# Kernel tuning notes

Hardware: AMD Instinct MI355X
Metric: run time of the kernel (lower is better)

Reference implementation:

```python
import jax, jax.numpy as jnp
import numpy as np

B, SEQ, PRED, DM = 16, 2048, 2048, 64
P = SEQ + PRED            # PointNum = 4096, per-node feature length
NLAYER, HID = 3, 4096     # MLPNums, ggdmodel hidden sizes
NH, HS = 16, 4096         # NumAttentionHeads, HiddenSize
G_CONST, K = 1.0, 8
NN = DM * DM              # 4096 == P, MHSA input dim (required by original code)


def setup_inputs() -> dict:
    key = jax.random.key(0)
    ks = jax.random.split(key, 11)
    s_mlp = 1.0 / np.sqrt(P).astype(np.float32)
    s_att = 1.0 / np.sqrt(NN).astype(np.float32)
    s_out = 1.0 / np.sqrt(HS).astype(np.float32)
    return {
        "x": jax.random.normal(ks[0], (B, P, DM), jnp.float32),
        "W_mlp": jax.random.normal(ks[1], (NLAYER, P, HID), jnp.float32) * s_mlp,
        "b_mlp": jnp.zeros((NLAYER, HID), jnp.float32),
        "Wq": jax.random.normal(ks[2], (NN, HS), jnp.float32) * s_att,
        "bq": jnp.zeros((HS,), jnp.float32),
        "Wk": jax.random.normal(ks[3], (NN, HS), jnp.float32) * s_att,
        "bk": jnp.zeros((HS,), jnp.float32),
        "Wv": jax.random.normal(ks[4], (NN, HS), jnp.float32) * s_att,
        "bv": jnp.zeros((HS,), jnp.float32),
        "Wo": jax.random.normal(ks[5], (HS, HS), jnp.float32) * s_out,
        "bo": jnp.zeros((HS,), jnp.float32),
    }


def _grav_adj(h):
    # h: [B, N, D] node features -> symmetrized, top-K masked gravity adjacency [B, N, N]
    norm = jnp.linalg.norm(h, axis=-1)                      # [B, N]
    m = jnp.sum(h, axis=-1) / norm                          # node "mass"
    sim = jnp.einsum('bnd,bmd->bnm', h, h) / (norm[:, :, None] * norm[:, None, :])
    F = G_CONST * m[:, :, None] * m[:, None, :] * sim * sim  # gravity matrix
    kth = jax.lax.top_k(F, K)[0][..., -1:]                  # per-row Kth largest value
    F = jnp.where(F >= kth, F, 0.0)                         # keep only top-K per row
    F = jnp.maximum(F, 0.0)                                 # ReLU
    return 0.5 * (F + jnp.swapaxes(F, -1, -2))              # symmetrize


def reference(x, W_mlp, b_mlp, Wq, bq, Wk, bk, Wv, bv, Wo, bo):
    h = jnp.swapaxes(x, 1, 2)                               # [B, N=DM, P]
    adjs = [_grav_adj(h)]
    for l in range(NLAYER):                                 # each MLP applied to the same h
        hv = h @ W_mlp[l] + b_mlp[l]                        # [B, N, HID]
        adjs.append(_grav_adj(hv))
    A = jnp.stack(adjs, axis=1)                             # [B, L, N, N], L = NLAYER + 1
    Lseq = A.shape[1]
    tok = A.reshape(B, Lseq, NN)                            # L tokens of dim N*N
    dh = HS // NH
    q = (tok @ Wq + bq).reshape(B, Lseq, NH, dh)
    k = (tok @ Wk + bk).reshape(B, Lseq, NH, dh)
    v = (tok @ Wv + bv).reshape(B, Lseq, NH, dh)
    scores = jnp.einsum('blhd,bmhd->bhlm', q, k) / np.sqrt(dh).astype(np.float32)
    attn = jax.nn.softmax(scores, axis=-1)
    ctx = jnp.einsum('bhlm,bmhd->blhd', attn, v).reshape(B, Lseq, HS)
    out = ctx @ Wo + bo                                     # [B, L, HS]
    return jnp.where(out > 0.5, out, 0.0)
```

## Files before the change

kernel.cpp:

```cpp
#include <hip/hip_runtime.h>
#include <math.h>


#define B16 16
#define PDIM 4096
#define NNODE 64
#define NCHUNK 32
#define KCG 128

typedef __attribute__((ext_vector_type(8))) short bf16x8;
typedef __attribute__((ext_vector_type(4))) float f32x4;
typedef __attribute__((ext_vector_type(4))) unsigned short us4;
typedef __attribute__((ext_vector_type(8))) unsigned short us8;

__device__ inline void split2(float x, unsigned short& h, unsigned short& l) {
  unsigned u = __float_as_uint(x);
  unsigned hu = (u + 0x7fffu + ((u >> 16) & 1u)) & 0xffff0000u;
  h = (unsigned short)(hu >> 16);
  float lo = x - __uint_as_float(hu);
  unsigned u2 = __float_as_uint(lo);
  l = (unsigned short)((u2 + 0x7fffu + ((u2 >> 16) & 1u)) >> 16);
}

__device__ inline void gload16(const void* g, void* lds) {
  __builtin_amdgcn_global_load_lds((const unsigned int*)g, (unsigned int*)lds, 16, 0, 0);
}

__global__ __launch_bounds__(256) void k_transpose(const float* __restrict__ x,
                                                   float* __restrict__ h,
                                                   unsigned short* __restrict__ AhT,
                                                   unsigned short* __restrict__ AlT,
                                                   int mode) {
  __shared__ float t[64][65];
  int b = blockIdx.y;
  int p0 = blockIdx.x * 64;
  const float* xb = x + (size_t)b * PDIM * NNODE;
#pragma unroll
  for (int i = 0; i < 16; ++i) {
    int e = i * 256 + threadIdx.x;
    int p = e >> 6, n = e & 63;
    t[p][n] = xb[(size_t)p0 * 64 + e];
  }
  __syncthreads();
  if (mode != 2) {
    float* hb = h + (size_t)b * NNODE * PDIM;
#pragma unroll
    for (int i = 0; i < 16; ++i) {
      int e = i * 256 + threadIdx.x;
      int n = e >> 6, p = e & 63;
      hb[(size_t)n * PDIM + p0 + p] = t[p][n];
    }
  }
  if (mode == 0) return;
#pragma unroll
  for (int j = 0; j < 2; ++j) {
    int cid = j * 256 + threadIdx.x;
    int n2 = cid >> 3, kg8 = cid & 7;
    us8 hv_, lv_;
#pragma unroll
    for (int e = 0; e < 8; ++e) {
      unsigned short hh, ll;
      split2(t[kg8 * 8 + e][n2], hh, ll);
      hv_[e] = hh; lv_[e] = ll;
    }
    int m = b * 64 + n2;
    int ks = (p0 >> 5) + (kg8 >> 2);
    size_t idx = (((size_t)(m >> 7) * 128 + ks) * 8 + ((m >> 4) & 7)) * 512 +
                 (size_t)((n2 & 15) + 16 * (kg8 & 3)) * 8;
    *(us8*)&AhT[idx] = hv_;
    *(us8*)&AlT[idx] = lv_;
  }
}

__global__ __launch_bounds__(512) void k_gemm_mlpf(
    const unsigned short* __restrict__ Ah, const unsigned short* __restrict__ Al,
    const float* __restrict__ W, float* __restrict__ Cp) {
  __shared__ unsigned short sAh[2][4096], sAl[2][4096];
  __shared__ unsigned short sBh[2][4096], sBl[2][4096];
  int tid = threadIdx.x;
  int l = tid & 63, wid = tid >> 6;
  int wr = wid >> 2, wc = wid & 3;
  int nb = blockIdx.x, mb = blockIdx.y, z = blockIdx.z;
  const int spp = 64;
  int ks0 = z * spp;

  size_t abase = ((size_t)mb * 128 + ks0) * 4096 + tid * 8;

  const float* wbase = W + (size_t)((l >> 4) * 8) * 4096 + nb * 128 + wid * 16 + (l & 15);
  int sidx = wid * 512 + l * 8;

  f32x4 acc[4][2];
#pragma unroll
  for (int i = 0; i < 4; ++i)
#pragma unroll
    for (int j = 0; j < 2; ++j) acc[i][j] = (f32x4){0.f, 0.f, 0.f, 0.f};

  gload16(Ah + abase, &sAh[0][tid * 8]);
  gload16(Al + abase, &sAl[0][tid * 8]);
  {
    us8 hi, lo;
#pragma unroll
    for (int e = 0; e < 8; ++e) {
      unsigned short hh, ll;
      split2(wbase[(size_t)ks0 * 131072 + (size_t)e * 4096], hh, ll);
      hi[e] = hh; lo[e] = ll;
    }
    *(us8*)&sBh[0][sidx] = hi;
    *(us8*)&sBl[0][sidx] = lo;
  }
  __syncthreads();

  int buf = 0;
  for (int t = 0; t < spp; ++t) {
    bool more = (t + 1 < spp);
    float wv[8];
    if (more) {
      size_t off = abase + (size_t)(t + 1) * 4096;
      gload16(Ah + off, &sAh[buf ^ 1][tid * 8]);
      gload16(Al + off, &sAl[buf ^ 1][tid * 8]);
      size_t wo = (size_t)(ks0 + t + 1) * 131072;
#pragma unroll
      for (int e = 0; e < 8; ++e) wv[e] = wbase[wo + (size_t)e * 4096];
    }
    bf16x8 ah[4], al4[4], bh2[2], bl2[2];
#pragma unroll
    for (int i = 0; i < 4; ++i) {
      ah[i]  = *(const bf16x8*)&sAh[buf][(wr * 4 + i) * 512 + l * 8];
      al4[i] = *(const bf16x8*)&sAl[buf][(wr * 4 + i) * 512 + l * 8];
    }
#pragma unroll
    for (int j = 0; j < 2; ++j) {
      bh2[j] = *(const bf16x8*)&sBh[buf][(wc * 2 + j) * 512 + l * 8];
      bl2[j] = *(const bf16x8*)&sBl[buf][(wc * 2 + j) * 512 + l * 8];
    }
#pragma unroll
    for (int mt = 0; mt < 4; ++mt)
#pragma unroll
      for (int nt = 0; nt < 2; ++nt) {
        acc[mt][nt] = __builtin_amdgcn_mfma_f32_16x16x32_bf16(ah[mt],  bh2[nt], acc[mt][nt], 0, 0, 0);
        acc[mt][nt] = __builtin_amdgcn_mfma_f32_16x16x32_bf16(ah[mt],  bl2[nt], acc[mt][nt], 0, 0, 0);
        acc[mt][nt] = __builtin_amdgcn_mfma_f32_16x16x32_bf16(al4[mt], bh2[nt], acc[mt][nt], 0, 0, 0);
      }
    if (more) {
      us8 hi, lo;
#pragma unroll
      for (int e = 0; e < 8; ++e) {
        unsigned short hh, ll;
        split2(wv[e], hh, ll);
        hi[e] = hh; lo[e] = ll;
      }
      *(us8*)&sBh[buf ^ 1][sidx] = hi;
      *(us8*)&sBl[buf ^ 1][sidx] = lo;
    }
    __syncthreads();
    buf ^= 1;
  }

  int n0 = nb * 128, m0 = mb * 128;
  float* Cz = Cp + (size_t)z * 4194304;
#pragma unroll
  for (int mt = 0; mt < 4; ++mt)
#pragma unroll
    for (int nt = 0; nt < 2; ++nt) {
      int col = n0 + wc * 32 + nt * 16 + (l & 15);
      int rowb = m0 + wr * 64 + mt * 16 + ((l >> 4) << 2);
#pragma unroll
      for (int r = 0; r < 4; ++r)
        Cz[(size_t)(rowb + r) * 4096 + col] = acc[mt][nt][r];
    }
}

__global__ __launch_bounds__(512) void k_gemm_wsf32(
    const unsigned short* __restrict__ Ah, const unsigned short* __restrict__ Al,
    const float* __restrict__ W0, const float* __restrict__ W1,
    const float* __restrict__ W2, float* __restrict__ Cp, int ksplit) {
  __shared__ unsigned short sAh[2][2048], sAl[2][2048];
  __shared__ unsigned short sBh[2][4096], sBl[2][4096];
  int tid = threadIdx.x;
  int l = tid & 63, wid = tid >> 6;
  int wr = wid >> 2, wc = wid & 3;
  int nb = blockIdx.x, z = blockIdx.z;
  int mat = z / ksplit, kz = z - mat * ksplit;
  const float* W = (mat == 0) ? W0 : ((mat == 1) ? W1 : W2);
  int nsteps = 128 / ksplit;
  int ks0 = kz * nsteps;
  int n0 = nb * 128;

  const float* wbase = W + (size_t)((l >> 4) * 8) * 4096 + n0 + wid * 16 + (l & 15);
  int sidx = wid * 512 + l * 8;

  f32x4 acc[2][2];
#pragma unroll
  for (int i = 0; i < 2; ++i)
#pragma unroll
    for (int j = 0; j < 2; ++j) acc[i][j] = (f32x4){0.f, 0.f, 0.f, 0.f};

  {
    if (tid < 256) gload16(Ah + (size_t)ks0 * 4096 + tid * 8, &sAh[0][tid * 8]);
    else           gload16(Al + (size_t)ks0 * 4096 + (tid - 256) * 8, &sAl[0][(tid - 256) * 8]);
    float wv[8];
#pragma unroll
    for (int e = 0; e < 8; ++e) wv[e] = wbase[(size_t)ks0 * 131072 + (size_t)e * 4096];
    us8 hi, lo;
#pragma unroll
    for (int e = 0; e < 8; ++e) {
      unsigned short hh, ll;
      split2(wv[e], hh, ll);
      hi[e] = hh; lo[e] = ll;
    }
    *(us8*)&sBh[0][sidx] = hi;
    *(us8*)&sBl[0][sidx] = lo;
  }
  __syncthreads();

  int buf = 0;
  for (int t = 0; t < nsteps; ++t) {
    bool more = (t + 1 < nsteps);
    float wv[8];
    if (more) {
      int ks = ks0 + t + 1;
      if (tid < 256) gload16(Ah + (size_t)ks * 4096 + tid * 8, &sAh[buf ^ 1][tid * 8]);
      else           gload16(Al + (size_t)ks * 4096 + (tid - 256) * 8, &sAl[buf ^ 1][(tid - 256) * 8]);
#pragma unroll
      for (int e = 0; e < 8; ++e) wv[e] = wbase[(size_t)ks * 131072 + (size_t)e * 4096];
    }
    bf16x8 aH[2], aL[2], bH[2], bL[2];
#pragma unroll
    for (int i = 0; i < 2; ++i) {
      aH[i] = *(const bf16x8*)&sAh[buf][(wr * 2 + i) * 512 + l * 8];
      aL[i] = *(const bf16x8*)&sAl[buf][(wr * 2 + i) * 512 + l * 8];
      bH[i] = *(const bf16x8*)&sBh[buf][(wc * 2 + i) * 512 + l * 8];
      bL[i] = *(const bf16x8*)&sBl[buf][(wc * 2 + i) * 512 + l * 8];
    }
#pragma unroll
    for (int i = 0; i < 2; ++i)
#pragma unroll
      for (int j = 0; j < 2; ++j) {
        acc[i][j] = __builtin_amdgcn_mfma_f32_16x16x32_bf16(aH[i], bH[j], acc[i][j], 0, 0, 0);
        acc[i][j] = __builtin_amdgcn_mfma_f32_16x16x32_bf16(aH[i], bL[j], acc[i][j], 0, 0, 0);
        acc[i][j] = __builtin_amdgcn_mfma_f32_16x16x32_bf16(aL[i], bH[j], acc[i][j], 0, 0, 0);
      }
    if (more) {
      us8 hi, lo;
#pragma unroll
      for (int e = 0; e < 8; ++e) {
        unsigned short hh, ll;
        split2(wv[e], hh, ll);
        hi[e] = hh; lo[e] = ll;
      }
      *(us8*)&sBh[buf ^ 1][sidx] = hi;
      *(us8*)&sBl[buf ^ 1][sidx] = lo;
    }
    __syncthreads();
    buf ^= 1;
  }

  float* Cz = Cp + (size_t)z * 262144;
#pragma unroll
  for (int i = 0; i < 2; ++i)
#pragma unroll
    for (int j = 0; j < 2; ++j) {
      int col = n0 + wc * 32 + j * 16 + (l & 15);
#pragma unroll
      for (int r = 0; r < 4; ++r) {
        int row = (wr * 2 + i) * 16 + ((l >> 4) << 2) + r;
        Cz[(size_t)row * 4096 + col] = acc[i][j][r];
      }
    }
}

__global__ __launch_bounds__(256) void k_gram_fuse(
    const float* __restrict__ Cp, const float* __restrict__ bias,
    float* __restrict__ Gp, float* __restrict__ Sp, int nparts) {
  __shared__ unsigned short sZh[2048], sZl[2048];
  int zk = blockIdx.x, b = blockIdx.y;
  int tid = threadIdx.x;
  int l = tid & 63, w = tid >> 6;
  int srow = tid >> 2, skq = tid & 3;
  const float* cbase = Cp + (size_t)(b * 64 + srow) * 4096;
  int swidx = (srow >> 4) * 512 + (skq * 16 + (srow & 15)) * 8;

  f32x4 acc[4], racc;
#pragma unroll
  for (int j = 0; j < 4; ++j) acc[j] = (f32x4){0.f, 0.f, 0.f, 0.f};
  racc = (f32x4){0.f, 0.f, 0.f, 0.f};
  bf16x8 ones;
#pragma unroll
  for (int e = 0; e < 8; ++e) ones[e] = (short)0x3F80;

  for (int s = 0; s < 8; ++s) {
    int k0 = zk * 256 + s * 32 + skq * 8;
    float v[8];
#pragma unroll
    for (int e = 0; e < 8; ++e) v[e] = bias[k0 + e];
    for (int p = 0; p < nparts; ++p) {
      const float* pp = cbase + (size_t)p * 4194304 + k0;
      float4 a0 = *(const float4*)pp;
      float4 a1 = *(const float4*)(pp + 4);
      v[0] += a0.x; v[1] += a0.y; v[2] += a0.z; v[3] += a0.w;
      v[4] += a1.x; v[5] += a1.y; v[6] += a1.z; v[7] += a1.w;
    }
    us8 hi, lo;
#pragma unroll
    for (int e = 0; e < 8; ++e) {
      unsigned short hh, ll;
      split2(v[e], hh, ll);
      hi[e] = hh; lo[e] = ll;
    }
    *(us8*)&sZh[swidx] = hi;
    *(us8*)&sZl[swidx] = lo;
    __syncthreads();
    bf16x8 bh[4], bl4[4];
#pragma unroll
    for (int nt = 0; nt < 4; ++nt) {
      bh[nt]  = *(const bf16x8*)&sZh[nt * 512 + l * 8];
      bl4[nt] = *(const bf16x8*)&sZl[nt * 512 + l * 8];
    }
    bf16x8 ah = bh[w], al = bl4[w];
#pragma unroll
    for (int nt = 0; nt < 4; ++nt) {
      acc[nt] = __builtin_amdgcn_mfma_f32_16x16x32_bf16(ah, bh[nt], acc[nt], 0, 0, 0);
      acc[nt] = __builtin_amdgcn_mfma_f32_16x16x32_bf16(ah, bl4[nt], acc[nt], 0, 0, 0);
      acc[nt] = __builtin_amdgcn_mfma_f32_16x16x32_bf16(al, bh[nt], acc[nt], 0, 0, 0);
    }
    racc = __builtin_amdgcn_mfma_f32_16x16x32_bf16(ah, ones, racc, 0, 0, 0);
    racc = __builtin_amdgcn_mfma_f32_16x16x32_bf16(al, ones, racc, 0, 0, 0);
    __syncthreads();
  }

  float* Gz = Gp + ((size_t)zk * B16 + b) * 4096;
#pragma unroll
  for (int nt = 0; nt < 4; ++nt) {
    int col = nt * 16 + (l & 15);
#pragma unroll
    for (int r = 0; r < 4; ++r) {
      int row = w * 16 + ((l >> 4) << 2) + r;
      Gz[row * 64 + col] = acc[nt][r];
    }
  }
  if ((l & 15) == 0) {
    float* Sz = Sp + ((size_t)zk * B16 + b) * 64;
#pragma unroll
    for (int r = 0; r < 4; ++r) Sz[w * 16 + ((l >> 4) << 2) + r] = racc[r];
  }
}

__global__ __launch_bounds__(256) void k_gram_mfma(
    const unsigned short* __restrict__ Zh, const unsigned short* __restrict__ Zl,
    float* __restrict__ Gp, float* __restrict__ Sp,
    int bs1, int ks_stride, int nsteps) {
  __shared__ unsigned short sZh[2][2048], sZl[2][2048];
  int z = blockIdx.x, b = blockIdx.y;
  int tid = threadIdx.x;
  int l = tid & 63, w = tid >> 6;
  size_t zbase = (size_t)(b >> 1) * 524288 + (size_t)(b & 1) * bs1;
  int ks0 = z * nsteps;

  f32x4 acc[4], racc;
#pragma unroll
  for (int j = 0; j < 4; ++j) acc[j] = (f32x4){0.f, 0.f, 0.f, 0.f};
  racc = (f32x4){0.f, 0.f, 0.f, 0.f};
  bf16x8 ones;
#pragma unroll
  for (int e = 0; e < 8; ++e) ones[e] = (short)0x3F80;

  gload16(Zh + zbase + (size_t)ks0 * ks_stride + tid * 8, &sZh[0][tid * 8]);
  gload16(Zl + zbase + (size_t)ks0 * ks_stride + tid * 8, &sZl[0][tid * 8]);
  __syncthreads();

  int buf = 0;
  for (int t = 0; t < nsteps; ++t) {
    if (t + 1 < nsteps) {
      size_t off = zbase + (size_t)(ks0 + t + 1) * ks_stride + tid * 8;
      gload16(Zh + off, &sZh[buf ^ 1][tid * 8]);
      gload16(Zl + off, &sZl[buf ^ 1][tid * 8]);
    }
    bf16x8 bh[4], bl4[4];
#pragma unroll
    for (int nt = 0; nt < 4; ++nt) {
      bh[nt]  = *(const bf16x8*)&sZh[buf][nt * 512 + l * 8];
      bl4[nt] = *(const bf16x8*)&sZl[buf][nt * 512 + l * 8];
    }
    bf16x8 ah = bh[w], al = bl4[w];
#pragma unroll
    for (int nt = 0; nt < 4; ++nt) {
      acc[nt] = __builtin_amdgcn_mfma_f32_16x16x32_bf16(ah, bh[nt], acc[nt], 0, 0, 0);
      acc[nt] = __builtin_amdgcn_mfma_f32_16x16x32_bf16(ah, bl4[nt], acc[nt], 0, 0, 0);
      acc[nt] = __builtin_amdgcn_mfma_f32_16x16x32_bf16(al, bh[nt], acc[nt], 0, 0, 0);
    }
    racc = __builtin_amdgcn_mfma_f32_16x16x32_bf16(ah, ones, racc, 0, 0, 0);
    racc = __builtin_amdgcn_mfma_f32_16x16x32_bf16(al, ones, racc, 0, 0, 0);
    __syncthreads();
    buf ^= 1;
  }

  float* Gz = Gp + ((size_t)z * B16 + b) * 4096;
#pragma unroll
  for (int nt = 0; nt < 4; ++nt) {
    int col = nt * 16 + (l & 15);
#pragma unroll
    for (int r = 0; r < 4; ++r) {
      int row = w * 16 + ((l >> 4) << 2) + r;
      Gz[row * 64 + col] = acc[nt][r];
    }
  }
  if ((l & 15) == 0) {
    float* Sz = Sp + ((size_t)z * B16 + b) * 64;
#pragma unroll
    for (int r = 0; r < 4; ++r) Sz[w * 16 + ((l >> 4) << 2) + r] = racc[r];
  }
}

__global__ __launch_bounds__(256) void k_gred(const float* __restrict__ Gp,
                                              const float* __restrict__ Sp,
                                              float* __restrict__ G,
                                              float* __restrict__ S, int slot, int nc) {
  int idx = blockIdx.x * 256 + threadIdx.x;
  if (idx < 65536) {
    float s = 0.f;
    for (int c = 0; c < nc; ++c) s += Gp[(size_t)c * 65536 + idx];
    G[(size_t)slot * 65536 + idx] = s;
  } else if (idx < 66560) {
    int i2 = idx - 65536;
    float s = 0.f;
    for (int c = 0; c < nc; ++c) s += Sp[(size_t)c * 1024 + i2];
    S[(size_t)slot * 1024 + i2] = s;
  }
}

__global__ __launch_bounds__(256) void k_redqkv8(const float* __restrict__ Cp,
                                                 const float* __restrict__ bq,
                                                 const float* __restrict__ bk,
                                                 const float* __restrict__ bv,
                                                 float* __restrict__ q,
                                                 float* __restrict__ k,
                                                 float* __restrict__ v) {
  int idx = blockIdx.x * 256 + threadIdx.x;
  int mat = idx >> 18;
  int rn = idx & ((1 << 18) - 1);
  int n = rn & 4095;
  const float* base = Cp + (size_t)mat * 8 * 262144;
  float s = 0.f;
#pragma unroll
  for (int p = 0; p < 8; ++p) s += base[(size_t)p * 262144 + rn];
  if (mat == 0) q[rn] = s + bq[n];
  else if (mat == 1) k[rn] = s + bk[n];
  else v[rn] = s + bv[n];
}

__global__ __launch_bounds__(256) void k_redN(const float* __restrict__ Cp,
                                              const float* __restrict__ bias,
                                              float* __restrict__ dst,
                                              int nparts, int thr) {
  int idx = blockIdx.x * 256 + threadIdx.x;
  float s = bias[idx & 4095];
  for (int p = 0; p < nparts; ++p) s += Cp[(size_t)p * 262144 + idx];
  if (thr) s = (s > 0.5f) ? s : 0.f;
  dst[idx] = s;
}

__device__ inline float wmax64(float v) {
#pragma unroll
  for (int off = 32; off; off >>= 1) v = fmaxf(v, __shfl_xor(v, off));
  return v;
}

__global__ __launch_bounds__(256) void k_adj_t(const float* __restrict__ G,
                                               const float* __restrict__ S,
                                               unsigned short* __restrict__ tokh,
                                               unsigned short* __restrict__ tokl) {
  __shared__ float Fm[64][64];
  __shared__ float nrm[64], mm[64];
  int b = blockIdx.x >> 2, lz = blockIdx.x & 3;
  int tid = threadIdx.x;
  int j = tid & 63, w = tid >> 6;
  const float* Gb = G + ((size_t)lz * B16 + b) * 4096;
  const float* Sb = S + ((size_t)lz * B16 + b) * 64;
  if (tid < 64) {
    float nj = sqrtf(Gb[tid * 64 + tid]);
    nrm[tid] = nj;
    mm[tid] = Sb[tid] / nj;
  }
  __syncthreads();
  for (int i = w; i < 64; i += 4) {
    float g = Gb[i * 64 + j];
    float sim = g / (nrm[i] * nrm[j]);
    Fm[i][j] = mm[i] * mm[j] * sim * sim;
  }
  __syncthreads();
  for (int i = w; i < 64; i += 4) {
    float f = Fm[i][j];
    int cnt = 0;
#pragma unroll
    for (int u4 = 0; u4 < 16; ++u4) {
      float4 q = *(const float4*)&Fm[i][u4 * 4];
      cnt += (q.x > f) + (q.y > f) + (q.z > f) + (q.w > f);
    }
    float cand = (cnt <= 7) ? f : INFINITY;
#pragma unroll
    for (int off = 32; off; off >>= 1) cand = fminf(cand, __shfl_xor(cand, off));
    float fm = (f >= cand) ? fmaxf(f, 0.f) : 0.f;
    Fm[i][j] = fm;
  }
  __syncthreads();
  int r = b * 4 + lz;
  int mt = r >> 4, rl = r & 15;
#pragma unroll
  for (int c = 0; c < 2; ++c) {
    int cid = tid * 2 + c;
    int jj0 = cid >> 3, g = cid & 7;
    us8 hv_, lv_;
#pragma unroll
    for (int e = 0; e < 8; ++e) {
      int kcol = g * 8 + e;
      float val = 0.5f * (Fm[jj0][kcol] + Fm[kcol][jj0]);
      unsigned short hh, ll;
      split2(val, hh, ll);
      hv_[e] = hh; lv_[e] = ll;
    }
    int ks = jj0 * 2 + (g >> 2);
    size_t idx = ((size_t)ks * 8 + mt) * 512 + (size_t)(rl + 16 * (g & 3)) * 8;
    *(us8*)&tokh[idx] = hv_;
    *(us8*)&tokl[idx] = lv_;
  }
}

__global__ __launch_bounds__(64) void k_attn_t(const float* __restrict__ q,
                                               const float* __restrict__ k,
                                               const float* __restrict__ v,
                                               unsigned short* __restrict__ ctxh,
                                               unsigned short* __restrict__ ctxl) {
  __shared__ float cb[4][256];
  int hd = blockIdx.x, b = blockIdx.y;
  int t = threadIdx.x;
  float qr[4][4], kr[4][4], vr[4][4];
#pragma unroll
  for (int l = 0; l < 4; ++l)
#pragma unroll
    for (int s = 0; s < 4; ++s) {
      size_t off = ((size_t)(b * 4 + l)) * 4096 + hd * 256 + t + s * 64;
      qr[l][s] = q[off]; kr[l][s] = k[off]; vr[l][s] = v[off];
    }
  float sc[4][4];
#pragma unroll
  for (int l = 0; l < 4; ++l)
#pragma unroll
    for (int m = 0; m < 4; ++m) {
      float p = 0.f;
#pragma unroll
      for (int s = 0; s < 4; ++s) p = fmaf(qr[l][s], kr[m][s], p);
#pragma unroll
      for (int off = 32; off; off >>= 1) p += __shfl_xor(p, off);
      sc[l][m] = p * (1.0f / 16.0f);
    }
  float at[4][4];
#pragma unroll
  for (int l = 0; l < 4; ++l) {
    float mx = fmaxf(fmaxf(sc[l][0], sc[l][1]), fmaxf(sc[l][2], sc[l][3]));
    float e0 = expf(sc[l][0] - mx), e1 = expf(sc[l][1] - mx);
    float e2 = expf(sc[l][2] - mx), e3 = expf(sc[l][3] - mx);
    float d = e0 + e1 + e2 + e3;
    at[l][0] = e0 / d; at[l][1] = e1 / d; at[l][2] = e2 / d; at[l][3] = e3 / d;
  }
#pragma unroll
  for (int l = 0; l < 4; ++l)
#pragma unroll
    for (int s = 0; s < 4; ++s) {
      float c = 0.f;
#pragma unroll
      for (int m = 0; m < 4; ++m) c = fmaf(at[l][m], vr[m][s], c);
      cb[l][s * 64 + t] = c;
    }
  __syncthreads();
  int lq = t >> 4, c16 = t & 15;
  int mt = b >> 2, rl = (b & 3) * 4 + lq;
#pragma unroll
  for (int e8 = 0; e8 < 2; ++e8) {
    us8 hv_, lv_;
#pragma unroll
    for (int e = 0; e < 8; ++e) {
      unsigned short hh, ll;
      split2(cb[lq][c16 * 16 + e8 * 8 + e], hh, ll);
      hv_[e] = hh; lv_[e] = ll;
    }
    int ks = hd * 8 + (c16 >> 1);
    size_t idx = ((size_t)ks * 8 + mt) * 512 + (size_t)(rl + 16 * ((c16 * 2 + e8) & 3)) * 8;
    *(us8*)&ctxh[idx] = hv_;
    *(us8*)&ctxl[idx] = lv_;
  }
}

__global__ __launch_bounds__(256) void k_gram_partial(const float* __restrict__ Z,
                                                      float* __restrict__ Gp,
                                                      float* __restrict__ Sp) {
  __shared__ float Zt[KCG][68];
  int c = blockIdx.x, b = blockIdx.y;
  int tid = threadIdx.x;
  const float* Zb = Z + (size_t)b * NNODE * PDIM + c * KCG;
#pragma unroll
  for (int i = 0; i < 32; ++i) {
    int e = i * 256 + tid;
    int r = e >> 7, kk = e & 127;
    Zt[kk][r] = Zb[(size_t)r * PDIM + kk];
  }
  __syncthreads();
  int ii = tid >> 2, j0 = (tid & 3) << 4;
  float acc[16] = {};
  for (int kk = 0; kk < KCG; ++kk) {
    float zi = Zt[kk][ii];
    float4 z0 = *(const float4*)&Zt[kk][j0 + 0];
    float4 z1 = *(const float4*)&Zt[kk][j0 + 4];
    float4 z2 = *(const float4*)&Zt[kk][j0 + 8];
    float4 z3 = *(const float4*)&Zt[kk][j0 + 12];
    acc[0] = fmaf(zi, z0.x, acc[0]);   acc[1] = fmaf(zi, z0.y, acc[1]);
    acc[2] = fmaf(zi, z0.z, acc[2]);   acc[3] = fmaf(zi, z0.w, acc[3]);
    acc[4] = fmaf(zi, z1.x, acc[4]);   acc[5] = fmaf(zi, z1.y, acc[5]);
    acc[6] = fmaf(zi, z1.z, acc[6]);   acc[7] = fmaf(zi, z1.w, acc[7]);
    acc[8] = fmaf(zi, z2.x, acc[8]);   acc[9] = fmaf(zi, z2.y, acc[9]);
    acc[10] = fmaf(zi, z2.z, acc[10]); acc[11] = fmaf(zi, z2.w, acc[11]);
    acc[12] = fmaf(zi, z3.x, acc[12]); acc[13] = fmaf(zi, z3.y, acc[13]);
    acc[14] = fmaf(zi, z3.z, acc[14]); acc[15] = fmaf(zi, z3.w, acc[15]);
  }
  float* gp = Gp + ((size_t)c * B16 + b) * 4096 + ii * 64 + j0;
#pragma unroll
  for (int j = 0; j < 16; ++j) gp[j] = acc[j];
  if (tid < 64) {
    float s = 0.f;
    for (int kk = 0; kk < KCG; ++kk) s += Zt[kk][tid];
    Sp[((size_t)c * B16 + b) * 64 + tid] = s;
  }
}

__global__ __launch_bounds__(256) void k_gram_reduce(const float* __restrict__ Gp,
                                                     const float* __restrict__ Sp,
                                                     float* __restrict__ G,
                                                     float* __restrict__ S, int slot) {
  int idx = blockIdx.x * 256 + threadIdx.x;
  if (idx < B16 * 4096) {
    float s = 0.f;
    for (int c = 0; c < NCHUNK; ++c) s += Gp[(size_t)c * (B16 * 4096) + idx];
    G[(size_t)slot * (B16 * 4096) + idx] = s;
  } else {
    int idx2 = idx - B16 * 4096;
    float s = 0.f;
    for (int c = 0; c < NCHUNK; ++c) s += Sp[(size_t)c * (B16 * 64) + idx2];
    S[(size_t)slot * (B16 * 64) + idx2] = s;
  }
}

__global__ __launch_bounds__(256) void k_gemm_mfma(
    const float* __restrict__ A, const float* __restrict__ B0,
    const float* __restrict__ B1, const float* __restrict__ B2,
    const float* __restrict__ bias, float* __restrict__ C,
    int mrows, int mstore, int N, int K, int ksplit) {
  __shared__ __align__(16) unsigned short sA[2][8][64][8];
  __shared__ __align__(16) unsigned short sB[2][8][64][8];
  int z = blockIdx.z;
  int mat = z / ksplit, ks = z - mat * ksplit;
  const float* Bm = (mat == 0) ? B0 : ((mat == 1) ? B1 : B2);
  int kchunk = K / ksplit;
  int k0 = ks * kchunk, k1 = k0 + kchunk;
  int tid = threadIdx.x;
  int l = tid & 63;
  int wr = (tid >> 7) & 1, wc = (tid >> 6) & 1;
  int m0 = blockIdx.y * 128, n0g = blockIdx.x * 128;
  bool activeM = (m0 + wr * 64) < mstore;
  int am = tid >> 1;
  int arow = m0 + am; if (arow >= mrows) arow = mrows - 1;
  const float* Arow = A + (size_t)arow * K;
  int amt = am >> 4;
  int bk = tid >> 3;
  int bnb = (tid & 7) * 4;
  int bg = bk >> 3, bslot = bk & 7;
  f32x4 acc[4][4];
#pragma unroll
  for (int i = 0; i < 4; ++i)
#pragma unroll
    for (int j = 0; j < 4; ++j) acc[i][j] = (f32x4){0.f, 0.f, 0.f, 0.f};
  for (int kb = k0; kb < k1; kb += 32) {
    __syncthreads();
#pragma unroll
    for (int i = 0; i < 4; ++i) {
      int kq = (tid & 1) * 4 + i * 8;
      float4 a = *(const float4*)(Arow + kb + kq);
      unsigned short h0, h1, h2, h3, l0, l1, l2, l3;
      split2(a.x, h0, l0); split2(a.y, h1, l1);
      split2(a.z, h2, l2); split2(a.w, h3, l3);
      int lane_t = (am & 15) + 16 * (kq >> 3);
      int sb = kq & 4;
      *(us4*)&sA[0][amt][lane_t][sb] = (us4){h0, h1, h2, h3};
      *(us4*)&sA[1][amt][lane_t][sb] = (us4){l0, l1, l2, l3};
    }
    {
      const float* Brow = Bm + (size_t)(kb + bk) * N + n0g;
#pragma unroll
      for (int i = 0; i < 4; ++i) {
        int n = bnb + i * 32;
        int nt = n >> 4, nr = n & 15;
        float4 b = *(const float4*)(Brow + n);
        float be[4] = {b.x, b.y, b.z, b.w};
#pragma unroll
        for (int e = 0; e < 4; ++e) {
          unsigned short hh, ll;
          split2(be[e], hh, ll);
          sB[0][nt][nr + e + 16 * bg][bslot] = hh;
          sB[1][nt][nr + e + 16 * bg][bslot] = ll;
        }
      }
    }
    __syncthreads();
    if (!activeM) continue;
    bf16x8 ah[4], al[4], bh[4], bl[4];
#pragma unroll
    for (int t = 0; t < 4; ++t) {
      ah[t] = *(const bf16x8*)&sA[0][wr * 4 + t][l][0];
      al[t] = *(const bf16x8*)&sA[1][wr * 4 + t][l][0];
      bh[t] = *(const bf16x8*)&sB[0][wc * 4 + t][l][0];
      bl[t] = *(const bf16x8*)&sB[1][wc * 4 + t][l][0];
    }
#pragma unroll
    for (int mt = 0; mt < 4; ++mt)
#pragma unroll
      for (int nt = 0; nt < 4; ++nt) {
        acc[mt][nt] = __builtin_amdgcn_mfma_f32_16x16x32_bf16(ah[mt], bh[nt], acc[mt][nt], 0, 0, 0);
        acc[mt][nt] = __builtin_amdgcn_mfma_f32_16x16x32_bf16(ah[mt], bl[nt], acc[mt][nt], 0, 0, 0);
        acc[mt][nt] = __builtin_amdgcn_mfma_f32_16x16x32_bf16(al[mt], bh[nt], acc[mt][nt], 0, 0, 0);
      }
  }
  if (!activeM) return;
  float* Cz = C + (size_t)z * mstore * N;
#pragma unroll
  for (int mt = 0; mt < 4; ++mt)
#pragma unroll
    for (int nt = 0; nt < 4; ++nt) {
      int col = n0g + wc * 64 + nt * 16 + (l & 15);
      float badd = bias ? bias[col] : 0.f;
#pragma unroll
      for (int r = 0; r < 4; ++r) {
        int row = m0 + wr * 64 + mt * 16 + ((l >> 4) << 2) + r;
        if (row < mstore) Cz[(size_t)row * N + col] = acc[mt][nt][r] + badd;
      }
    }
}

__global__ __launch_bounds__(64) void k_adj_fb(const float* __restrict__ G,
                                               const float* __restrict__ S,
                                               float* __restrict__ tok) {
  __shared__ float Fm[64][64];
  __shared__ float nrm[64], mm[64];
  int b = blockIdx.x >> 2, lz = blockIdx.x & 3;
  int j = threadIdx.x;
  const float* Gb = G + ((size_t)lz * B16 + b) * 4096;
  const float* Sb = S + ((size_t)lz * B16 + b) * 64;
  float nj = sqrtf(Gb[j * 64 + j]);
  nrm[j] = nj;
  mm[j] = Sb[j] / nj;
  __syncthreads();
  for (int i = 0; i < 64; ++i) {
    float g = Gb[i * 64 + j];
    float sim = g / (nrm[i] * nj);
    float F = mm[i] * mm[j] * sim * sim;
    float v = F;
    bool act = true;
    float kth = 0.f;
#pragma unroll
    for (int it = 0; it < 8; ++it) {
      float mv = wmax64(act ? v : -INFINITY);
      kth = mv;
      unsigned long long ball = __ballot(act && (v == mv));
      int first = __ffsll(ball) - 1;
      if (j == first) act = false;
    }
    float fm = (F >= kth) ? F : 0.f;
    Fm[i][j] = fmaxf(fm, 0.f);
  }
  __syncthreads();
  float* tb = tok + ((size_t)b * 4 + lz) * 4096;
  for (int i = 0; i < 64; ++i) tb[i * 64 + j] = 0.5f * (Fm[i][j] + Fm[j][i]);
}

__global__ __launch_bounds__(256) void k_qkv_reduce(const float* __restrict__ Cp,
                                                    const float* __restrict__ bq,
                                                    const float* __restrict__ bk,
                                                    const float* __restrict__ bv,
                                                    float* __restrict__ q,
                                                    float* __restrict__ k,
                                                    float* __restrict__ v) {
  int idx = blockIdx.x * 256 + threadIdx.x;
  int mat = idx >> 18;
  int rn = idx & ((1 << 18) - 1);
  int n = rn & 4095;
  const float* base = Cp + (size_t)mat * 4 * 262144;
  float s = base[rn] + base[rn + 262144] + base[rn + 2 * 262144] + base[rn + 3 * 262144];
  if (mat == 0) q[rn] = s + bq[n];
  else if (mat == 1) k[rn] = s + bk[n];
  else v[rn] = s + bv[n];
}

__global__ __launch_bounds__(64) void k_attn_fb(const float* __restrict__ q,
                                                const float* __restrict__ k,
                                                const float* __restrict__ v,
                                                float* __restrict__ ctx) {
  int hd = blockIdx.x, b = blockIdx.y;
  int t = threadIdx.x;
  float qr[4][4], kr[4][4], vr[4][4];
#pragma unroll
  for (int l = 0; l < 4; ++l)
#pragma unroll
    for (int s = 0; s < 4; ++s) {
      size_t off = ((size_t)(b * 4 + l)) * 4096 + hd * 256 + t + s * 64;
      qr[l][s] = q[off]; kr[l][s] = k[off]; vr[l][s] = v[off];
    }
  float sc[4][4];
#pragma unroll
  for (int l = 0; l < 4; ++l)
#pragma unroll
    for (int m = 0; m < 4; ++m) {
      float p = 0.f;
#pragma unroll
      for (int s = 0; s < 4; ++s) p = fmaf(qr[l][s], kr[m][s], p);
#pragma unroll
      for (int off = 32; off; off >>= 1) p += __shfl_xor(p, off);
      sc[l][m] = p * (1.0f / 16.0f);
    }
  float at[4][4];
#pragma unroll
  for (int l = 0; l < 4; ++l) {
    float mx = fmaxf(fmaxf(sc[l][0], sc[l][1]), fmaxf(sc[l][2], sc[l][3]));
    float e0 = expf(sc[l][0] - mx), e1 = expf(sc[l][1] - mx);
    float e2 = expf(sc[l][2] - mx), e3 = expf(sc[l][3] - mx);
    float d = e0 + e1 + e2 + e3;
    at[l][0] = e0 / d; at[l][1] = e1 / d; at[l][2] = e2 / d; at[l][3] = e3 / d;
  }
#pragma unroll
  for (int l = 0; l < 4; ++l)
#pragma unroll
    for (int s = 0; s < 4; ++s) {
      float c = 0.f;
#pragma unroll
      for (int m = 0; m < 4; ++m) c = fmaf(at[l][m], vr[m][s], c);
      ctx[((size_t)(b * 4 + l)) * 4096 + hd * 256 + t + s * 64] = c;
    }
}

__global__ __launch_bounds__(256) void k_out_reduce(const float* __restrict__ Cp,
                                                    const float* __restrict__ bo,
                                                    float* __restrict__ out) {
  int idx = blockIdx.x * 256 + threadIdx.x;
  int n = idx & 4095;
  float s = bo[n];
#pragma unroll
  for (int p = 0; p < 8; ++p) s += Cp[(size_t)p * 262144 + idx];
  out[idx] = (s > 0.5f) ? s : 0.f;
}

extern "C" void kernel_launch(void* const* d_in, const int* in_sizes, int n_in,
                              void* d_out, int out_size, void* d_ws, size_t ws_size,
                              hipStream_t stream) {
  const float* x     = (const float*)d_in[0];
  const float* W_mlp = (const float*)d_in[1];
  const float* b_mlp = (const float*)d_in[2];
  const float* Wq = (const float*)d_in[3]; const float* bq = (const float*)d_in[4];
  const float* Wk = (const float*)d_in[5]; const float* bk = (const float*)d_in[6];
  const float* Wv = (const float*)d_in[7]; const float* bv = (const float*)d_in[8];
  const float* Wo = (const float*)d_in[9]; const float* bo = (const float*)d_in[10];
  float* out = (float*)d_out;
  float* ws = (float*)d_ws;

  float* h   = ws;
  float* Gp  = ws + 8388608;
  float* Sp  = ws + 10485760;
  float* G   = ws + 10518528;
  float* S   = ws + 10780672;

  const size_t NEED = 50368512ull * 4ull;
  if (ws_size >= NEED) {
    float* q   = ws + 10784768;
    float* kk  = ws + 11046912;
    float* vv  = ws + 11309056;
    unsigned short* AhT = (unsigned short*)(ws + 11571200);
    unsigned short* AlT = (unsigned short*)(ws + 13668352);
    float* Cp           = ws + 32542720;
    unsigned short* tokh = (unsigned short*)(ws + 49319936);
    unsigned short* tokl = (unsigned short*)(ws + 49582080);
    unsigned short* ctxh = (unsigned short*)(ws + 49844224);
    unsigned short* ctxl = (unsigned short*)(ws + 50106368);

    k_transpose<<<dim3(64, 16), 256, 0, stream>>>(x, h, AhT, AlT, 2);

    k_gram_mfma<<<dim3(8, 16), 256, 0, stream>>>(AhT, AlT, Gp, Sp, 2048, 4096, 16);
    k_gred<<<260, 256, 0, stream>>>(Gp, Sp, G, S, 0, 8);

    for (int l = 0; l < 3; ++l) {
      k_gemm_mlpf<<<dim3(32, 8, 2), 512, 0, stream>>>(AhT, AlT,
                                                      W_mlp + (size_t)l * 16777216, Cp);
      k_gram_fuse<<<dim3(16, 16), 256, 0, stream>>>(Cp, b_mlp + (size_t)l * 4096,
                                                    Gp, Sp, 2);
      k_gred<<<260, 256, 0, stream>>>(Gp, Sp, G, S, l + 1, 16);
    }

    k_adj_t<<<64, 256, 0, stream>>>(G, S, tokh, tokl);

    k_gemm_wsf32<<<dim3(32, 1, 24), 512, 0, stream>>>(tokh, tokl, Wq, Wk, Wv, Cp, 8);
    k_redqkv8<<<3072, 256, 0, stream>>>(Cp, bq, bk, bv, q, kk, vv);

    k_attn_t<<<dim3(16, 16), 64, 0, stream>>>(q, kk, vv, ctxh, ctxl);

    k_gemm_wsf32<<<dim3(32, 1, 8), 512, 0, stream>>>(ctxh, ctxl, Wo, Wo, Wo, Cp, 8);
    k_redN<<<1024, 256, 0, stream>>>(Cp, bo, out, 8, 1);
  } else {
    float* hv  = ws + 4194304;
    float* tok = ws + 10784768;
    float* q   = ws + 11046912;
    float* kk  = ws + 11309056;
    float* vv  = ws + 11571200;
    float* ctx = ws + 11833344;
    float* qkvp = hv;
    float* op   = h;

    k_transpose<<<dim3(64, 16), 256, 0, stream>>>(x, h, (unsigned short*)0,
                                                  (unsigned short*)0, 0);
    k_gram_partial<<<dim3(NCHUNK, 16), 256, 0, stream>>>(h, Gp, Sp);
    k_gram_reduce<<<260, 256, 0, stream>>>(Gp, Sp, G, S, 0);
    for (int l = 0; l < 3; ++l) {
      const float* Wl = W_mlp + (size_t)l * PDIM * 4096;
      const float* bl = b_mlp + (size_t)l * 4096;
      k_gemm_mfma<<<dim3(32, 8, 1), 256, 0, stream>>>(h, Wl, Wl, Wl, bl, hv,
                                                      1024, 1024, 4096, 4096, 1);
      k_gram_partial<<<dim3(NCHUNK, 16), 256, 0, stream>>>(hv, Gp, Sp);
      k_gram_reduce<<<260, 256, 0, stream>>>(Gp, Sp, G, S, l + 1);
    }
    k_adj_fb<<<64, 64, 0, stream>>>(G, S, tok);
    k_gemm_mfma<<<dim3(32, 1, 12), 256, 0, stream>>>(tok, Wq, Wk, Wv, nullptr, qkvp,
                                                     64, 64, 4096, 4096, 4);
    k_qkv_reduce<<<3072, 256, 0, stream>>>(qkvp, bq, bk, bv, q, kk, vv);
    k_attn_fb<<<dim3(16, 16), 64, 0, stream>>>(q, kk, vv, ctx);
    k_gemm_mfma<<<dim3(32, 1, 8), 256, 0, stream>>>(ctx, Wo, Wo, Wo, nullptr, op,
                                                    64, 64, 4096, 4096, 8);
    k_out_reduce<<<1024, 256, 0, stream>>>(op, bo, out);
  }
}
```

Baseline: 593.1 us.

## Pre-split MLP weights into bf16 hi/lo tiles before a pure-async GEMM

Adds a separate k_wsplit kernel that converts each MLP weight matrix into pre-tiled bf16 hi/lo arrays. The GEMM can then stream both operands with async global-to-LDS loads instead of doing strided fp32 loads and splitting them inside the main loop. This removes conversion ALU work and register-staged B loads from the GEMM critical path. The cost is an extra pass per layer that reads 64MB of fp32 and writes 64MB of bf16, with the GEMM then reading that 64MB again.

```diff
diff --git a/kernel.cpp b/kernel.cpp
--- a/kernel.cpp
+++ b/kernel.cpp
@@ -72,22 +72,53 @@
   }
 }
 
-__global__ __launch_bounds__(512) void k_gemm_mlpf(
+__global__ __launch_bounds__(256) void k_wsplit(const float* __restrict__ W,
+                                                unsigned short* __restrict__ WhT,
+                                                unsigned short* __restrict__ WlT) {
+  __shared__ float Wt[32][132];
+  int nb = blockIdx.x, kb = blockIdx.y;
+  int tid = threadIdx.x;
+#pragma unroll
+  for (int i = 0; i < 4; ++i) {
+    int idx = i * 256 + tid;
+    int row = idx >> 5, c4 = idx & 31;
+    float4 v = *(const float4*)&W[(size_t)(kb * 32 + row) * 4096 + nb * 128 + c4 * 4];
+    *(float4*)&Wt[row][c4 * 4] = v;
+  }
+  __syncthreads();
+#pragma unroll
+  for (int j = 0; j < 2; ++j) {
+    int cid = j * 256 + tid;
+    int nl = cid & 127, kg = cid >> 7;
+    us8 hv_, lv_;
+#pragma unroll
+    for (int e = 0; e < 8; ++e) {
+      unsigned short hh, ll;
+      split2(Wt[kg * 8 + e][nl], hh, ll);
+      hv_[e] = hh; lv_[e] = ll;
+    }
+    size_t idx = (((size_t)nb * 128 + kb) * 8 + (nl >> 4)) * 512 +
+                 (size_t)((nl & 15) + 16 * kg) * 8;
+    *(us8*)&WhT[idx] = hv_;
+    *(us8*)&WlT[idx] = lv_;
+  }
+}
+
+__global__ __launch_bounds__(512) void k_gemm_bf16(
     const unsigned short* __restrict__ Ah, const unsigned short* __restrict__ Al,
-    const float* __restrict__ W, float* __restrict__ Cp) {
+    const unsigned short* __restrict__ Bh, const unsigned short* __restrict__ Bl,
+    float* __restrict__ Cp, int Ksteps, int ksplit, int N, int mstore) {
   __shared__ unsigned short sAh[2][4096], sAl[2][4096];
   __shared__ unsigned short sBh[2][4096], sBl[2][4096];
   int tid = threadIdx.x;
   int l = tid & 63, wid = tid >> 6;
   int wr = wid >> 2, wc = wid & 3;
   int nb = blockIdx.x, mb = blockIdx.y, z = blockIdx.z;
-  const int spp = 64;
+  int spp = Ksteps / ksplit;
   int ks0 = z * spp;
 
-  size_t abase = ((size_t)mb * 128 + ks0) * 4096 + tid * 8;
-
-  const float* wbase = W + (size_t)((l >> 4) * 8) * 4096 + nb * 128 + wid * 16 + (l & 15);
-  int sidx = wid * 512 + l * 8;
+  const size_t abase = ((size_t)mb * Ksteps + ks0) * 4096 + tid * 8;
+  const size_t bbase = ((size_t)nb * Ksteps + ks0) * 4096 + tid * 8;
 
   f32x4 acc[4][2];
 #pragma unroll
@@ -97,41 +128,29 @@
 
   gload16(Ah + abase, &sAh[0][tid * 8]);
   gload16(Al + abase, &sAl[0][tid * 8]);
-  {
-    us8 hi, lo;
-#pragma unroll
-    for (int e = 0; e < 8; ++e) {
-      unsigned short hh, ll;
-      split2(wbase[(size_t)ks0 * 131072 + (size_t)e * 4096], hh, ll);
-      hi[e] = hh; lo[e] = ll;
-    }
-    *(us8*)&sBh[0][sidx] = hi;
-    *(us8*)&sBl[0][sidx] = lo;
-  }
+  gload16(Bh + bbase, &sBh[0][tid * 8]);
+  gload16(Bl + bbase, &sBl[0][tid * 8]);
   __syncthreads();
 
   int buf = 0;
   for (int t = 0; t < spp; ++t) {
-    bool more = (t + 1 < spp);
-    float wv[8];
-    if (more) {
-      size_t off = abase + (size_t)(t + 1) * 4096;
-      gload16(Ah + off, &sAh[buf ^ 1][tid * 8]);
-      gload16(Al + off, &sAl[buf ^ 1][tid * 8]);
-      size_t wo = (size_t)(ks0 + t + 1) * 131072;
-#pragma unroll
-      for (int e = 0; e < 8; ++e) wv[e] = wbase[wo + (size_t)e * 4096];
+    if (t + 1 < spp) {
+      size_t off = (size_t)(t + 1) * 4096;
+      gload16(Ah + abase + off, &sAh[buf ^ 1][tid * 8]);
+      gload16(Al + abase + off, &sAl[buf ^ 1][tid * 8]);
+      gload16(Bh + bbase + off, &sBh[buf ^ 1][tid * 8]);
+      gload16(Bl + bbase + off, &sBl[buf ^ 1][tid * 8]);
     }
     bf16x8 ah[4], al4[4], bh2[2], bl2[2];
 #pragma unroll
-    for (int i = 0; i < 4; ++i) {
-      ah[i]  = *(const bf16x8*)&sAh[buf][(wr * 4 + i) * 512 + l * 8];
-      al4[i] = *(const bf16x8*)&sAl[buf][(wr * 4 + i) * 512 + l * 8];
-    }
-#pragma unroll
-    for (int j = 0; j < 2; ++j) {
-      bh2[j] = *(const bf16x8*)&sBh[buf][(wc * 2 + j) * 512 + l * 8];
-      bl2[j] = *(const bf16x8*)&sBl[buf][(wc * 2 + j) * 512 + l * 8];
+    for (int mt = 0; mt < 4; ++mt) {
+      ah[mt]  = *(const bf16x8*)&sAh[buf][(wr * 4 + mt) * 512 + l * 8];
+      al4[mt] = *(const bf16x8*)&sAl[buf][(wr * 4 + mt) * 512 + l * 8];
+    }
+#pragma unroll
+    for (int nt = 0; nt < 2; ++nt) {
+      bh2[nt] = *(const bf16x8*)&sBh[buf][(wc * 2 + nt) * 512 + l * 8];
+      bl2[nt] = *(const bf16x8*)&sBl[buf][(wc * 2 + nt) * 512 + l * 8];
     }
 #pragma unroll
     for (int mt = 0; mt < 4; ++mt)
@@ -141,32 +160,22 @@
         acc[mt][nt] = __builtin_amdgcn_mfma_f32_16x16x32_bf16(ah[mt],  bl2[nt], acc[mt][nt], 0, 0, 0);
         acc[mt][nt] = __builtin_amdgcn_mfma_f32_16x16x32_bf16(al4[mt], bh2[nt], acc[mt][nt], 0, 0, 0);
       }
-    if (more) {
-      us8 hi, lo;
-#pragma unroll
-      for (int e = 0; e < 8; ++e) {
-        unsigned short hh, ll;
-        split2(wv[e], hh, ll);
-        hi[e] = hh; lo[e] = ll;
-      }
-      *(us8*)&sBh[buf ^ 1][sidx] = hi;
-      *(us8*)&sBl[buf ^ 1][sidx] = lo;
-    }
     __syncthreads();
     buf ^= 1;
   }
 
   int n0 = nb * 128, m0 = mb * 128;
-  float* Cz = Cp + (size_t)z * 4194304;
+  float* Cz = Cp + (size_t)z * mstore * N;
 #pragma unroll
   for (int mt = 0; mt < 4; ++mt)
 #pragma unroll
     for (int nt = 0; nt < 2; ++nt) {
       int col = n0 + wc * 32 + nt * 16 + (l & 15);
-      int rowb = m0 + wr * 64 + mt * 16 + ((l >> 4) << 2);
-#pragma unroll
-      for (int r = 0; r < 4; ++r)
-        Cz[(size_t)(rowb + r) * 4096 + col] = acc[mt][nt][r];
+#pragma unroll
+      for (int r = 0; r < 4; ++r) {
+        int row = m0 + wr * 64 + mt * 16 + ((l >> 4) << 2) + r;
+        if (row < mstore) Cz[(size_t)row * N + col] = acc[mt][nt][r];
+      }
     }
 }
 
@@ -880,6 +889,8 @@
     float* vv  = ws + 11309056;
     unsigned short* AhT = (unsigned short*)(ws + 11571200);
     unsigned short* AlT = (unsigned short*)(ws + 13668352);
+    unsigned short* WhT = (unsigned short*)(ws + 15765504);
+    unsigned short* WlT = (unsigned short*)(ws + 24154112);
     float* Cp           = ws + 32542720;
     unsigned short* tokh = (unsigned short*)(ws + 49319936);
     unsigned short* tokl = (unsigned short*)(ws + 49582080);
@@ -892,8 +903,9 @@
     k_gred<<<260, 256, 0, stream>>>(Gp, Sp, G, S, 0, 8);
 
     for (int l = 0; l < 3; ++l) {
-      k_gemm_mlpf<<<dim3(32, 8, 2), 512, 0, stream>>>(AhT, AlT,
-                                                      W_mlp + (size_t)l * 16777216, Cp);
+      k_wsplit<<<dim3(32, 128), 256, 0, stream>>>(W_mlp + (size_t)l * 16777216, WhT, WlT);
+      k_gemm_bf16<<<dim3(32, 8, 2), 512, 0, stream>>>(AhT, AlT, WhT, WlT, Cp,
+                                                      128, 2, 4096, 1024);
       k_gram_fuse<<<dim3(16, 16), 256, 0, stream>>>(Cp, b_mlp + (size_t)l * 4096,
                                                     Gp, Sp, 2);
       k_gred<<<260, 256, 0, stream>>>(Gp, Sp, G, S, l + 1, 16);
```

Result: faster. 559.0 us (-5.8%).
